# Kernel tuning notes

Hardware: AMD Instinct MI355X
Metric: run time of the kernel (lower is better)

## Reference

```python
import jax, jax.numpy as jnp
import numpy as np

N_U = 50000
N_I = 50000
E = 800000
HID = 64
HEADS = 4
OUT = 32
NEG_SLOPE = 0.2


def _gat(xs, xd, e, ws, wd, a_s, a_d, b, heads, ch, n_dst, concat):
    # xs:[Ns,Fin] xd:[Nd,Fin] e:[2,E]; PyG GATConv (no self loops, eval mode)
    hs = (xs @ ws).reshape(-1, heads, ch)  # [Ns,H,C]
    hd = (xd @ wd).reshape(-1, heads, ch)  # [Nd,H,C]
    al_s = jnp.einsum('nhc,hc->nh', hs, a_s)  # [Ns,H]
    al_d = jnp.einsum('nhc,hc->nh', hd, a_d)  # [Nd,H]
    src, dst = e[0], e[1]
    alpha = jax.nn.leaky_relu(al_s[src] + al_d[dst], NEG_SLOPE)  # [E,H]
    m = jax.lax.stop_gradient(jax.ops.segment_max(alpha, dst, num_segments=n_dst))
    ealpha = jnp.exp(alpha - m[dst])
    denom = jax.ops.segment_sum(ealpha, dst, num_segments=n_dst)
    coef = ealpha / (denom[dst] + 1e-16)  # segment softmax over incoming edges
    msg = hs[src] * coef[:, :, None]  # [E,H,C]
    out = jax.ops.segment_sum(msg, dst, num_segments=n_dst)  # [Nd,H,C]
    out = out.reshape(n_dst, heads * ch) if concat else out.mean(axis=1)
    return out + b


def _forward(x_user, x_item, e_u2i, e_i2u,
             p_user_w, p_user_b, p_item_w, p_item_b,
             l0_u2i_ws, l0_u2i_wd, l0_u2i_as, l0_u2i_ad, l0_u2i_b,
             l0_i2u_ws, l0_i2u_wd, l0_i2u_as, l0_i2u_ad, l0_i2u_b,
             l1_u2i_ws, l1_u2i_wd, l1_u2i_as, l1_u2i_ad, l1_u2i_b,
             l1_i2u_ws, l1_i2u_wd, l1_i2u_as, l1_i2u_ad, l1_i2u_b):
    hu = jax.nn.elu(x_user @ p_user_w + p_user_b)
    hi = jax.nn.elu(x_item @ p_item_w + p_item_b)
    # layer 0: heads=4, concat=True, out dim HID*HEADS; HeteroConv sum (one edge type per dst)
    hi1 = _gat(hu, hi, e_u2i, l0_u2i_ws, l0_u2i_wd, l0_u2i_as, l0_u2i_ad, l0_u2i_b, HEADS, HID, N_I, True)
    hu1 = _gat(hi, hu, e_i2u, l0_i2u_ws, l0_i2u_wd, l0_i2u_as, l0_i2u_ad, l0_i2u_b, HEADS, HID, N_U, True)
    hu1 = jax.nn.elu(hu1)  # dropout is identity in eval mode
    hi1 = jax.nn.elu(hi1)
    # layer 1: heads=1, concat=False -> mean over heads
    hi2 = _gat(hu1, hi1, e_u2i, l1_u2i_ws, l1_u2i_wd, l1_u2i_as, l1_u2i_ad, l1_u2i_b, 1, OUT, N_I, False)
    hu2 = _gat(hi1, hu1, e_i2u, l1_i2u_ws, l1_i2u_wd, l1_i2u_as, l1_i2u_ad, l1_i2u_b, 1, OUT, N_U, False)
    return hu2, hi2


def setup_inputs() -> dict:
    key = jax.random.key(0)
    ks = jax.random.split(key, 32)
    s = 0.1
    d = {
        'x_user': jax.random.normal(ks[0], (N_U, 128), jnp.float32),
        'x_item': jax.random.normal(ks[1], (N_I, 128), jnp.float32),
        'e_u2i': jax.random.randint(ks[2], (2, E), 0, 50000, jnp.int32),
        'e_i2u': jax.random.randint(ks[3], (2, E), 0, 50000, jnp.int32),
        'p_user_w': jax.random.normal(ks[4], (128, HID), jnp.float32) * s,
        'p_user_b': jax.random.normal(ks[5], (HID,), jnp.float32) * s,
        'p_item_w': jax.random.normal(ks[6], (128, HID), jnp.float32) * s,
        'p_item_b': jax.random.normal(ks[7], (HID,), jnp.float32) * s,
    }
    i = 8
    for lname, fin, h, c in (('l0', HID, HEADS, HID), ('l1', HID * HEADS, 1, OUT)):
        for et in ('u2i', 'i2u'):
            odim = h * c if lname == 'l0' else c
            d[f'{lname}_{et}_ws'] = jax.random.normal(ks[i], (fin, h * c), jnp.float32) * s; i += 1
            d[f'{lname}_{et}_wd'] = jax.random.normal(ks[i], (fin, h * c), jnp.float32) * s; i += 1
            d[f'{lname}_{et}_as'] = jax.random.normal(ks[i], (h, c), jnp.float32) * s; i += 1
            d[f'{lname}_{et}_ad'] = jax.random.normal(ks[i], (h, c), jnp.float32) * s; i += 1
            d[f'{lname}_{et}_b'] = jax.random.normal(ks[i], (odim,), jnp.float32) * s; i += 1
    return d


def reference(x_user, x_item, e_u2i, e_i2u,
              p_user_w, p_user_b, p_item_w, p_item_b,
              l0_u2i_ws, l0_u2i_wd, l0_u2i_as, l0_u2i_ad, l0_u2i_b,
              l0_i2u_ws, l0_i2u_wd, l0_i2u_as, l0_i2u_ad, l0_i2u_b,
              l1_u2i_ws, l1_u2i_wd, l1_u2i_as, l1_u2i_ad, l1_u2i_b,
              l1_i2u_ws, l1_i2u_wd, l1_i2u_as, l1_i2u_ad, l1_i2u_b):
    return _forward(x_user, x_item, e_u2i, e_i2u,
                    p_user_w, p_user_b, p_item_w, p_item_b,
                    l0_u2i_ws, l0_u2i_wd, l0_u2i_as, l0_u2i_ad, l0_u2i_b,
                    l0_i2u_ws, l0_i2u_wd, l0_i2u_as, l0_i2u_ad, l0_i2u_b,
                    l1_u2i_ws, l1_u2i_wd, l1_u2i_as, l1_u2i_ad, l1_u2i_b,
                    l1_i2u_ws, l1_i2u_wd, l1_i2u_as, l1_i2u_ad, l1_i2u_b)
```

## Files before the change

### kernel.cpp

```cpp
#include <hip/hip_runtime.h>
#include <cstdint>
#include <cstddef>

#define NN 50000
#define NE 800000
#define GB 196
#define TILE1 4096
#define CAP 8192

typedef __attribute__((ext_vector_type(8))) short short8;
typedef __attribute__((ext_vector_type(4))) float floatx4;

__device__ __forceinline__ float lrelu_f(float x){ return x >= 0.f ? x : 0.2f*x; }
__device__ __forceinline__ float elu_f(float x){ return x > 0.f ? x : __expf(x) - 1.f; }

__device__ __forceinline__ unsigned short f2bf(float f){
  unsigned int u = __float_as_uint(f);
  u += 0x7FFFu + ((u >> 16) & 1u);
  return (unsigned short)(u >> 16);
}
__device__ __forceinline__ float bf2f(unsigned int us){
  return __uint_as_float(us << 16);
}
__device__ __forceinline__ float4 bf4_load(const unsigned short* p){
  uint2 q = *(const uint2*)p;
  return make_float4(bf2f(q.x & 0xffffu), bf2f(q.x >> 16),
                     bf2f(q.y & 0xffffu), bf2f(q.y >> 16));
}
__device__ __forceinline__ uint2 bf4_pack(float4 o){
  uint2 p;
  p.x = (unsigned)f2bf(o.x) | ((unsigned)f2bf(o.y) << 16);
  p.y = (unsigned)f2bf(o.z) | ((unsigned)f2bf(o.w) << 16);
  return p;
}
__device__ __forceinline__ void split_bf(float a, unsigned short& h, unsigned short& l){
  h = f2bf(a);
  l = f2bf(a - bf2f(h));
}

__device__ __forceinline__ float dot2bf(float acc, unsigned a, unsigned b){
  asm("v_dot2_f32_bf16 %0, %1, %2, %0" : "+v"(acc) : "v"(a), "v"(b));
  return acc;
}

__device__ __forceinline__ void agg_pair(float (&acc)[4][8], float (&den)[4],
                                         uint4 q0, uint4 q1, uint2 w0, uint2 w1){
  const unsigned ONE2 = 0x3F803F80u;
  unsigned wp[4];
  wp[0] = __builtin_amdgcn_perm(w1.x, w0.x, 0x05040100u);
  wp[1] = __builtin_amdgcn_perm(w1.x, w0.x, 0x07060302u);
  wp[2] = __builtin_amdgcn_perm(w1.y, w0.y, 0x05040100u);
  wp[3] = __builtin_amdgcn_perm(w1.y, w0.y, 0x07060302u);
  unsigned xp[8];
  xp[0] = __builtin_amdgcn_perm(q1.x, q0.x, 0x05040100u);
  xp[1] = __builtin_amdgcn_perm(q1.x, q0.x, 0x07060302u);
  xp[2] = __builtin_amdgcn_perm(q1.y, q0.y, 0x05040100u);
  xp[3] = __builtin_amdgcn_perm(q1.y, q0.y, 0x07060302u);
  xp[4] = __builtin_amdgcn_perm(q1.z, q0.z, 0x05040100u);
  xp[5] = __builtin_amdgcn_perm(q1.z, q0.z, 0x07060302u);
  xp[6] = __builtin_amdgcn_perm(q1.w, q0.w, 0x05040100u);
  xp[7] = __builtin_amdgcn_perm(q1.w, q0.w, 0x07060302u);
  #pragma unroll
  for (int h=0;h<4;h++){
    den[h] = dot2bf(den[h], wp[h], ONE2);
    #pragma unroll
    for (int c=0;c<8;c++) acc[h][c] = dot2bf(acc[h][c], wp[h], xp[c]);
  }
}

__global__ __launch_bounds__(256) void ghist_kernel(const int* __restrict__ e0,
                                                    const int* __restrict__ e1,
                                                    int* __restrict__ ghist){
  const int ty = blockIdx.y;
  const int* e = ty ? e1 : e0;
  __shared__ int h[GB];
  for (int j=threadIdx.x; j<GB; j+=256) h[j]=0;
  __syncthreads();
  for (int i = blockIdx.x*256 + threadIdx.x; i < NE; i += 256*256)
    atomicAdd(&h[e[NE+i]>>8], 1);
  __syncthreads();
  for (int j=threadIdx.x; j<GB; j+=256) if (h[j]) atomicAdd(&ghist[ty*200+j], h[j]);
}

__global__ __launch_bounds__(256) void gscan_kernel(const int* __restrict__ ghist,
                                                    int* __restrict__ gbase,
                                                    int* __restrict__ gcur){
  __shared__ int wb[4];
  const int t = threadIdx.x, wv = t>>6, l = t&63;
  for (int ty=0; ty<2; ++ty){
    int v = (t < GB) ? ghist[ty*200+t] : 0;
    int sum = v;
    #pragma unroll
    for (int off=1; off<64; off<<=1){
      int x = __shfl_up(sum, off, 64);
      if (l >= off) sum += x;
    }
    if (l == 63) wb[wv] = sum;
    __syncthreads();
    int wbase = 0;
    #pragma unroll
    for (int w=0; w<4; ++w) if (w < wv) wbase += wb[w];
    int excl = wbase + sum - v;
    if (t <= GB) gbase[ty*200+t] = excl;
    if (t <  GB) gcur [ty*200+t] = excl;
    __syncthreads();
  }
}

__global__ __launch_bounds__(256) void part1_kernel(const int* __restrict__ e0,
                                                    const int* __restrict__ e1,
                                                    int* __restrict__ gcur,
                                                    int2* __restrict__ p0,
                                                    int2* __restrict__ p1){
  const int ty = blockIdx.y;
  const int* e = ty ? e1 : e0;
  int2* pairs = ty ? p1 : p0;
  __shared__ int cnt[256];
  __shared__ int lstart[256];
  __shared__ int lcur[256];
  __shared__ int curg[GB];
  __shared__ int lsrc[TILE1];
  __shared__ int ldst[TILE1];
  __shared__ int wb[4];
  const int t = threadIdx.x;
  cnt[t] = 0;
  __syncthreads();
  int dreg[16], sreg[16];
  const int base = blockIdx.x*TILE1;
  const int ntile = min(TILE1, NE - base);
  #pragma unroll
  for (int it=0; it<16; ++it){
    int i = base + it*256 + t;
    int d = -1, s = 0;
    if (i < NE){ d = e[NE+i]; s = e[i]; atomicAdd(&cnt[d>>8], 1); }
    dreg[it] = d; sreg[it] = s;
  }
  __syncthreads();
  int c = cnt[t], sum = c;
  #pragma unroll
  for (int off=1; off<64; off<<=1){
    int x = __shfl_up(sum, off, 64);
    if ((t&63) >= off) sum += x;
  }
  if ((t&63) == 63) wb[t>>6] = sum;
  __syncthreads();
  int wbase = 0;
  #pragma unroll
  for (int w=0; w<4; ++w) if (w < (t>>6)) wbase += wb[w];
  int excl = wbase + sum - c;
  lstart[t] = excl;
  lcur[t] = excl;
  if (t < GB && c > 0) curg[t] = atomicAdd(&gcur[ty*200+t], c);
  __syncthreads();
  #pragma unroll
  for (int it=0; it<16; ++it){
    int d = dreg[it];
    if (d >= 0){
      int pos = atomicAdd(&lcur[d>>8], 1);
      lsrc[pos] = sreg[it];
      ldst[pos] = d;
    }
  }
  __syncthreads();
  for (int i=t; i<ntile; i+=256){
    int d = ldst[i];
    int j = d>>8;
    pairs[curg[j] + (i - lstart[j])] = make_int2(lsrc[i], d);
  }
}

struct Part2Job {
  const int2* pairs; const int* gbase;
  const float* als; const float* ald;
  int* ssrc; int* offs; unsigned short* coef;
};
__global__ __launch_bounds__(256) void part2_kernel(Part2Job j0, Part2Job j1){
  const Part2Job jb = blockIdx.y ? j1 : j0;
  const int b = blockIdx.x;
  const int t = threadIdx.x;
  __shared__ int lcnt[256];
  __shared__ int lcur[256];
  __shared__ int wb[4];
  __shared__ int sorted_src[CAP];
  __shared__ unsigned char sorted_dl[CAP];
  const int gb0 = jb.gbase[b], gb1 = jb.gbase[b+1];
  const int n = gb1 - gb0;
  lcnt[t] = 0;
  __syncthreads();
  for (int i=t; i<n; i+=256)
    atomicAdd(&lcnt[jb.pairs[gb0+i].y - (b<<8)], 1);
  __syncthreads();
  int c = lcnt[t], sum = c;
  #pragma unroll
  for (int off=1; off<64; off<<=1){
    int x = __shfl_up(sum, off, 64);
    if ((t&63) >= off) sum += x;
  }
  if ((t&63) == 63) wb[t>>6] = sum;
  __syncthreads();
  int wbase = 0;
  #pragma unroll
  for (int w=0; w<4; ++w) if (w < (t>>6)) wbase += wb[w];
  int excl = wbase + sum - c;
  lcur[t] = excl;
  int g = (b<<8) + t;
  if (g <= NN) jb.offs[g] = gb0 + excl;
  __syncthreads();
  for (int i=t; i<n; i+=256){
    int2 pr = jb.pairs[gb0+i];
    int dl = pr.y - (b<<8);
    int pos = atomicAdd(&lcur[dl], 1);
    sorted_src[pos] = pr.x;
    sorted_dl[pos] = (unsigned char)dl;
  }
  __syncthreads();
  const float4* als4 = (const float4*)jb.als;
  const float4* ald4 = (const float4*)jb.ald;
  for (int i=t; i<n; i+=256){
    int s  = sorted_src[i];
    int dl = sorted_dl[i];
    float4 a  = als4[s];
    float4 ad = ald4[(b<<8)+dl];
    float4 w;
    w.x = __expf(lrelu_f(a.x+ad.x));
    w.y = __expf(lrelu_f(a.y+ad.y));
    w.z = __expf(lrelu_f(a.z+ad.z));
    w.w = __expf(lrelu_f(a.w+ad.w));
    ((uint2*)jb.coef)[gb0+i] = bf4_pack(w);
    jb.ssrc[gb0+i] = s;
  }
}

struct WcvJob {
  const float* W; const float* cwS; const float* cwD;
  unsigned short* Wth; unsigned short* Wtl;
  int K; int N; int mode;
};
struct WcvArgs { WcvJob j[6]; };
__global__ __launch_bounds__(256) void wconv_kernel(WcvArgs args){
  WcvJob jb = args.j[blockIdx.y];
  int idx = blockIdx.x*256 + threadIdx.x;
  if (idx >= jb.K * jb.N) return;
  int k = idx / jb.N, n = idx % jb.N;
  float val;
  if (jb.mode == 0) val = jb.W[(size_t)k*jb.N + n];
  else {
    if (n < 32)       val = jb.W[(size_t)k*32 + n];
    else if (n == 32) val = jb.cwS[k];
    else if (n == 33) val = jb.cwD[k];
    else              val = 0.f;
  }
  unsigned short h, g;
  split_bf(val, h, g);
  jb.Wth[(size_t)n*jb.K + k] = h;
  jb.Wtl[(size_t)n*jb.K + k] = g;
}

struct MgJob {
  const void* A;
  const unsigned short* Wth;
  const unsigned short* Wtl;
  const float* bias;
  void* C; float* outA; float* outB;
  const float* cwS; const float* cwD;
};
template<int NT, int KK, bool ELU, bool BF16OUT, bool BF16A, bool LG, bool LOGIT>
__global__ __launch_bounds__(256) void mgemm_kernel(MgJob j0, MgJob j1,
                                                    int M, int N)
{
  const MgJob jb = blockIdx.z ? j1 : j0;
  constexpr int TN = NT*16;
  __shared__ __align__(16) unsigned short Ah[64*72];
  __shared__ __align__(16) unsigned short Al[BF16A ? 8 : 64*72];
  __shared__ __align__(16) unsigned short Bh[TN*72];
  __shared__ __align__(16) unsigned short Bl[TN*72];
  __shared__ float CwS[LOGIT ? 256 : 1];
  __shared__ float CwD[LOGIT ? 256 : 1];
  const int t = threadIdx.x;
  const int m0 = blockIdx.x*64;
  const int n0 = blockIdx.y*TN;
  const int wv = t>>6, l = t&63;
  const int lr = l&15, lq = l>>4;
  if constexpr (LOGIT){ CwS[t] = jb.cwS[t]; CwD[t] = jb.cwD[t]; }
  floatx4 acc[NT];
  #pragma unroll
  for (int i=0;i<NT;i++) acc[i] = (floatx4){0.f,0.f,0.f,0.f};

  #pragma unroll
  for (int kt=0; kt<KK; kt+=64){
    if constexpr (BF16A){
      const unsigned short* A = (const unsigned short*)jb.A;
      #pragma unroll
      for (int i=0;i<2;i++){
        int li = t + i*256;
        int r = li >> 3, c8 = (li & 7)*8;
        short8 v = {0,0,0,0,0,0,0,0};
        if (m0 + r < M) v = *(const short8*)(A + (size_t)(m0+r)*KK + kt + c8);
        *(short8*)&Ah[r*72 + c8] = v;
      }
    } else {
      const float* A = (const float*)jb.A;
      #pragma unroll
      for (int i=0;i<4;i++){
        int li = t + i*256;
        int r = li >> 4, c4 = (li & 15)*4;
        float4 v = make_float4(0.f,0.f,0.f,0.f);
        if (m0 + r < M) v = *(const float4*)(A + (size_t)(m0+r)*KK + kt + c4);
        unsigned short h0,h1,h2,h3,g0,g1,g2,g3;
        split_bf(v.x,h0,g0); split_bf(v.y,h1,g1);
        split_bf(v.z,h2,g2); split_bf(v.w,h3,g3);
        uint2 ph = { (unsigned)h0 | ((unsigned)h1<<16), (unsigned)h2 | ((unsigned)h3<<16) };
        uint2 pl = { (unsigned)g0 | ((unsigned)g1<<16), (unsigned)g2 | ((unsigned)g3<<16) };
        *(uint2*)&Ah[r*72 + c4] = ph;
        *(uint2*)&Al[r*72 + c4] = pl;
      }
    }
    for (int c = t; c < TN*8; c += 256){
      int n  = c >> 3;
      int k8 = (c & 7) * 8;
      *(short8*)&Bh[n*72 + k8] =
          *(const short8*)(jb.Wth + (size_t)(n0 + n)*KK + kt + k8);
      *(short8*)&Bl[n*72 + k8] =
          *(const short8*)(jb.Wtl + (size_t)(n0 + n)*KK + kt + k8);
    }
    __syncthreads();
    #pragma unroll
    for (int ks=0; ks<2; ks++){
      const int koff = ks*32 + lq*8;
      short8 a_h = *(const short8*)&Ah[(wv*16+lr)*72 + koff];
      short8 a_l;
      if constexpr (!BF16A) a_l = *(const short8*)&Al[(wv*16+lr)*72 + koff];
      #pragma unroll
      for (int nt=0; nt<NT; nt++){
        short8 b_h = *(const short8*)&Bh[(nt*16+lr)*72 + koff];
        short8 b_l = *(const short8*)&Bl[(nt*16+lr)*72 + koff];
        acc[nt] = __builtin_amdgcn_mfma_f32_16x16x32_bf16(a_h, b_h, acc[nt], 0,0,0);
        acc[nt] = __builtin_amdgcn_mfma_f32_16x16x32_bf16(a_h, b_l, acc[nt], 0,0,0);
        if constexpr (!BF16A)
          acc[nt] = __builtin_amdgcn_mfma_f32_16x16x32_bf16(a_l, b_h, acc[nt], 0,0,0);
      }
    }
    __syncthreads();
  }
  float ls[LOGIT ? 4 : 1][LOGIT ? 4 : 1];
  float ld_[LOGIT ? 4 : 1][LOGIT ? 4 : 1];
  if constexpr (LOGIT){
    #pragma unroll
    for (int r=0;r<4;r++)
      #pragma unroll
      for (int h=0;h<4;h++){ ls[r][h]=0.f; ld_[r][h]=0.f; }
  }
  #pragma unroll
  for (int nt=0; nt<NT; nt++){
    int n = n0 + nt*16 + lr;
    float bv = jb.bias ? jb.bias[n] : 0.f;
    #pragma unroll
    for (int r=0;r<4;r++){
      int m = m0 + wv*16 + lq*4 + r;
      if (m < M){
        float o = acc[nt][r] + bv;
        if (ELU) o = elu_f(o);
        if constexpr (LG){
          if (n < 32)       ((unsigned short*)jb.C)[(size_t)m*32 + n] = f2bf(o);
          else if (n == 32) jb.outA[m] = o;
          else if (n == 33) jb.outB[m] = o;
        } else {
          if (BF16OUT) ((unsigned short*)jb.C)[(size_t)m*N + n] = f2bf(o);
          else         ((float*)jb.C)[(size_t)m*N + n] = o;
        }
        if constexpr (LOGIT){
          #pragma unroll
          for (int h=0;h<4;h++){
            ls[r][h]  = fmaf(o, CwS[h*64 + n], ls[r][h]);
            ld_[r][h] = fmaf(o, CwD[h*64 + n], ld_[r][h]);
          }
        }
      }
    }
  }
  if constexpr (LOGIT){
    #pragma unroll
    for (int r=0;r<4;r++)
      #pragma unroll
      for (int h=0;h<4;h++){
        float a = ls[r][h], d = ld_[r][h];
        #pragma unroll
        for (int off=1; off<16; off<<=1){
          a += __shfl_xor(a, off, 64);
          d += __shfl_xor(d, off, 64);
        }
        ls[r][h]=a; ld_[r][h]=d;
      }
    if (lr == 0){
      #pragma unroll
      for (int r=0;r<4;r++){
        int m = m0 + wv*16 + lq*4 + r;
        if (m < M){
          #pragma unroll
          for (int h=0;h<4;h++){
            jb.outA[(size_t)m*4 + h] = ls[r][h];
            jb.outB[(size_t)m*4 + h] = ld_[r][h];
          }
        }
      }
    }
  }
}

struct HgJob {
  const unsigned short* A;
  const unsigned short* Wth;
  const unsigned short* Wtl;
  const float* den;
  const float* bias; unsigned short* out;
};
__global__ __launch_bounds__(256) void hgemm_kernel(HgJob j0, HgJob j1){
  const HgJob jb = blockIdx.z ? j1 : j0;
  const int head = blockIdx.y;
  const int m0 = blockIdx.x*64;
  __shared__ __align__(16) unsigned short Ah[64*72];
  __shared__ __align__(16) unsigned short Bh[64*72];
  __shared__ __align__(16) unsigned short Bl[64*72];
  const int t = threadIdx.x;
  const int wv = t>>6, l = t&63;
  const int lr = l&15, lq = l>>4;
  floatx4 acc[4];
  #pragma unroll
  for (int i=0;i<4;i++) acc[i] = (floatx4){0.f,0.f,0.f,0.f};
  #pragma unroll
  for (int i=0;i<2;i++){
    int li = t + i*256;
    int r = li >> 3, c8 = (li & 7)*8;
    short8 v = {0,0,0,0,0,0,0,0};
    if (m0 + r < NN) v = *(const short8*)(jb.A + (size_t)(m0+r)*256 + head*64 + c8);
    *(short8*)&Ah[r*72 + c8] = v;
  }
  #pragma unroll
  for (int i=0;i<2;i++){
    int c  = t + i*256;
    int n  = c >> 3;
    int k8 = (c & 7) * 8;
    *(short8*)&Bh[n*72 + k8] =
        *(const short8*)(jb.Wth + (size_t)(head*64 + n)*64 + k8);
    *(short8*)&Bl[n*72 + k8] =
        *(const short8*)(jb.Wtl + (size_t)(head*64 + n)*64 + k8);
  }
  __syncthreads();
  #pragma unroll
  for (int ks=0; ks<2; ks++){
    const int koff = ks*32 + lq*8;
    short8 a_h = *(const short8*)&Ah[(wv*16+lr)*72 + koff];
    #pragma unroll
    for (int nt=0; nt<4; nt++){
      short8 b_h = *(const short8*)&Bh[(nt*16+lr)*72 + koff];
      short8 b_l = *(const short8*)&Bl[(nt*16+lr)*72 + koff];
      acc[nt] = __builtin_amdgcn_mfma_f32_16x16x32_bf16(a_h, b_h, acc[nt], 0,0,0);
      acc[nt] = __builtin_amdgcn_mfma_f32_16x16x32_bf16(a_h, b_l, acc[nt], 0,0,0);
    }
  }
  float inv[4];
  #pragma unroll
  for (int r=0;r<4;r++){
    int m = m0 + wv*16 + lq*4 + r;
    inv[r] = (m < NN) ? 1.f/(jb.den[(size_t)m*4 + head] + 1e-16f) : 0.f;
  }
  #pragma unroll
  for (int nt=0; nt<4; nt++){
    int col = head*64 + nt*16 + lr;
    float bv = jb.bias[col];
    #pragma unroll
    for (int r=0;r<4;r++){
      int m = m0 + wv*16 + lq*4 + r;
      if (m < NN)
        jb.out[(size_t)m*256 + col] = f2bf(elu_f(acc[nt][r]*inv[r] + bv));
    }
  }
}

struct CollapseJob { const float* W; const float* a; float* out; int K,H,C; };
struct CollapseArgs { CollapseJob j[8]; };
__global__ void collapse_kernel(CollapseArgs args){
  CollapseJob jb = args.j[blockIdx.x];
  int t = threadIdx.x;
  if (t < jb.K * jb.H){
    int k = t / jb.H, h = t % jb.H;
    const float* wr = jb.W + (size_t)k * (jb.H*jb.C) + h*jb.C;
    const float* ar = jb.a + h*jb.C;
    float s = 0.f;
    for (int c=0;c<jb.C;c++) s += wr[c]*ar[c];
    jb.out[h*jb.K + k] = s;
  }
}

struct AggPJob {
  const int* offs; const int* ssrc;
  const unsigned short* x;
  const unsigned short* coef;
  unsigned short* agg;
  float* den;
};
__global__ __launch_bounds__(256) void aggpre_kernel(AggPJob ja, AggPJob jbb){
  const AggPJob jb = blockIdx.y ? jbb : ja;
  const int tid = threadIdx.x;
  const int lane = tid & 63, wid = tid >> 6;
  const int grp = lane >> 3;
  const int cl  = lane & 7;
  const int c8  = cl * 8;
  const int dst = blockIdx.x*32 + wid*8 + grp;
  if (dst >= NN) return;
  const int b0 = jb.offs[dst], b1 = jb.offs[dst+1];
  float acc[4][8];
  float den[4] = {0.f,0.f,0.f,0.f};
  #pragma unroll
  for (int h=0;h<4;h++)
    #pragma unroll
    for (int c=0;c<8;c++) acc[h][c]=0.f;
  int e = b0;
  for (; e+3 < b1; e += 4){
    int s0 = jb.ssrc[e];
    int s1 = jb.ssrc[e+1];
    int s2 = jb.ssrc[e+2];
    int s3 = jb.ssrc[e+3];
    uint4 q0 = *(const uint4*)(jb.x + ((size_t)s0<<6) + c8);
    uint4 q1 = *(const uint4*)(jb.x + ((size_t)s1<<6) + c8);
    uint4 q2 = *(const uint4*)(jb.x + ((size_t)s2<<6) + c8);
    uint4 q3 = *(const uint4*)(jb.x + ((size_t)s3<<6) + c8);
    uint2 w0 = *(const uint2*)(jb.coef + (size_t)e*4);
    uint2 w1 = *(const uint2*)(jb.coef + (size_t)(e+1)*4);
    uint2 w2 = *(const uint2*)(jb.coef + (size_t)(e+2)*4);
    uint2 w3 = *(const uint2*)(jb.coef + (size_t)(e+3)*4);
    agg_pair(acc, den, q0, q1, w0, w1);
    agg_pair(acc, den, q2, q3, w2, w3);
  }
  if (e+1 < b1){
    int s0 = jb.ssrc[e];
    int s1 = jb.ssrc[e+1];
    uint4 q0 = *(const uint4*)(jb.x + ((size_t)s0<<6) + c8);
    uint4 q1 = *(const uint4*)(jb.x + ((size_t)s1<<6) + c8);
    uint2 w0 = *(const uint2*)(jb.coef + (size_t)e*4);
    uint2 w1 = *(const uint2*)(jb.coef + (size_t)(e+1)*4);
    agg_pair(acc, den, q0, q1, w0, w1);
    e += 2;
  }
  if (e < b1){
    int s = jb.ssrc[e];
    uint4 q = *(const uint4*)(jb.x + ((size_t)s<<6) + c8);
    uint2 w = *(const uint2*)(jb.coef + (size_t)e*4);
    float wf[4] = { bf2f(w.x & 0xffffu), bf2f(w.x >> 16),
                    bf2f(w.y & 0xffffu), bf2f(w.y >> 16) };
    float xf[8] = { bf2f(q.x & 0xffffu), bf2f(q.x >> 16),
                    bf2f(q.y & 0xffffu), bf2f(q.y >> 16),
                    bf2f(q.z & 0xffffu), bf2f(q.z >> 16),
                    bf2f(q.w & 0xffffu), bf2f(q.w >> 16) };
    #pragma unroll
    for (int h=0;h<4;h++){
      den[h] += wf[h];
      #pragma unroll
      for (int c=0;c<8;c++) acc[h][c] += wf[h]*xf[c];
    }
  }
  #pragma unroll
  for (int h=0;h<4;h++){
    uint2 plo = bf4_pack(make_float4(acc[h][0],acc[h][1],acc[h][2],acc[h][3]));
    uint2 phi = bf4_pack(make_float4(acc[h][4],acc[h][5],acc[h][6],acc[h][7]));
    uint4 pk = { plo.x, plo.y, phi.x, phi.y };
    *(uint4*)(jb.agg + (size_t)dst*256 + h*64 + c8) = pk;
  }
  if (cl == 0)
    *(float4*)(jb.den + (size_t)dst*4) = make_float4(den[0],den[1],den[2],den[3]);
}

struct Agg1Job {
  const int* offs; const int* ssrc;
  const unsigned short* hs;
  const float* als; const float* ald;
  const float* bias; float* out;
};
__global__ __launch_bounds__(256) void agg1_kernel(Agg1Job ja, Agg1Job jbb){
  const Agg1Job jb = blockIdx.y ? jbb : ja;
  const int wid = threadIdx.x>>6, lane = threadIdx.x&63;
  const int dst = blockIdx.x*4 + wid;
  if (dst >= NN) return;
  const int b0 = jb.offs[dst], b1 = jb.offs[dst+1];
  const float ad = jb.ald[dst];
  const int slot = lane>>3, c4 = (lane&7)*4;
  float4 acc = make_float4(0.f,0.f,0.f,0.f);
  float den = 0.f;
  int e = b0 + slot;
  for (; e+8 < b1; e += 16){
    int s0 = jb.ssrc[e], s1 = jb.ssrc[e+8];
    float a0 = jb.als[s0];
    float a1 = jb.als[s1];
    float4 v0 = bf4_load(jb.hs + ((size_t)s0<<5) + c4);
    float4 v1 = bf4_load(jb.hs + ((size_t)s1<<5) + c4);
    float w0 = __expf(lrelu_f(a0 + ad));
    float w1 = __expf(lrelu_f(a1 + ad));
    acc.x += w0*v0.x + w1*v1.x;
    acc.y += w0*v0.y + w1*v1.y;
    acc.z += w0*v0.z + w1*v1.z;
    acc.w += w0*v0.w + w1*v1.w;
    den += w0 + w1;
  }
  if (e < b1){
    int s = jb.ssrc[e];
    float w = __expf(lrelu_f(jb.als[s] + ad));
    float4 v = bf4_load(jb.hs + ((size_t)s<<5) + c4);
    acc.x += w*v.x; acc.y += w*v.y; acc.z += w*v.z; acc.w += w*v.w;
    den += w;
  }
  #pragma unroll
  for (int off=32; off>=8; off>>=1){
    acc.x += __shfl_xor(acc.x, off, 64);
    acc.y += __shfl_xor(acc.y, off, 64);
    acc.z += __shfl_xor(acc.z, off, 64);
    acc.w += __shfl_xor(acc.w, off, 64);
    den   += __shfl_xor(den,   off, 64);
  }
  if (lane < 8){
    const float inv = 1.f/(den + 1e-16f);
    float4 b = *(const float4*)(jb.bias + c4);
    float4 o = make_float4(acc.x*inv+b.x, acc.y*inv+b.y, acc.z*inv+b.z, acc.w*inv+b.w);
    *(float4*)(jb.out + (size_t)dst*32 + c4) = o;
  }
}

extern "C" void kernel_launch(void* const* d_in, const int* in_sizes, int n_in,
                              void* d_out, int out_size, void* d_ws, size_t ws_size,
                              hipStream_t stream)
{
  (void)in_sizes; (void)n_in; (void)out_size; (void)ws_size;
  const float* x_user   = (const float*)d_in[0];
  const float* x_item   = (const float*)d_in[1];
  const int*   e_u2i    = (const int*)  d_in[2];
  const int*   e_i2u    = (const int*)  d_in[3];
  const float* p_user_w = (const float*)d_in[4];
  const float* p_user_b = (const float*)d_in[5];
  const float* p_item_w = (const float*)d_in[6];
  const float* p_item_b = (const float*)d_in[7];
  const float* l0_u2i_ws=(const float*)d_in[8];
  const float* l0_u2i_wd=(const float*)d_in[9];
  const float* l0_u2i_as=(const float*)d_in[10];
  const float* l0_u2i_ad=(const float*)d_in[11];
  const float* l0_u2i_b =(const float*)d_in[12];
  const float* l0_i2u_ws=(const float*)d_in[13];
  const float* l0_i2u_wd=(const float*)d_in[14];
  const float* l0_i2u_as=(const float*)d_in[15];
  const float* l0_i2u_ad=(const float*)d_in[16];
  const float* l0_i2u_b =(const float*)d_in[17];
  const float* l1_u2i_ws=(const float*)d_in[18];
  const float* l1_u2i_wd=(const float*)d_in[19];
  const float* l1_u2i_as=(const float*)d_in[20];
  const float* l1_u2i_ad=(const float*)d_in[21];
  const float* l1_u2i_b =(const float*)d_in[22];
  const float* l1_i2u_ws=(const float*)d_in[23];
  const float* l1_i2u_wd=(const float*)d_in[24];
  const float* l1_i2u_as=(const float*)d_in[25];
  const float* l1_i2u_ad=(const float*)d_in[26];
  const float* l1_i2u_b =(const float*)d_in[27];

  char* base = (char*)d_ws;
  size_t off = 0;
  auto alloc = [&](size_t bytes)->void*{
    void* p = base + off;
    off += (bytes + 255) & ~(size_t)255;
    return p;
  };
  int* offs_u2i = (int*)alloc((size_t)(NN+1)*sizeof(int));
  int* offs_i2u = (int*)alloc((size_t)(NN+1)*sizeof(int));
  int* ssrc_u2i = (int*)alloc((size_t)NE*sizeof(int));
  int* ssrc_i2u = (int*)alloc((size_t)NE*sizeof(int));
  int* ghist    = (int*)alloc((size_t)2*200*sizeof(int));
  int* gbase    = (int*)alloc((size_t)2*200*sizeof(int));
  int* gcur     = (int*)alloc((size_t)2*200*sizeof(int));
  unsigned short* coef0_u2i = (unsigned short*)alloc((size_t)NE*4*sizeof(unsigned short));
  unsigned short* coef0_i2u = (unsigned short*)alloc((size_t)NE*4*sizeof(unsigned short));
  unsigned short* hu = (unsigned short*)alloc((size_t)NN*64*sizeof(unsigned short));
  unsigned short* hi = (unsigned short*)alloc((size_t)NN*64*sizeof(unsigned short));
  unsigned short* agg_u2i = (unsigned short*)alloc((size_t)NN*256*sizeof(unsigned short));
  unsigned short* agg_i2u = (unsigned short*)alloc((size_t)NN*256*sizeof(unsigned short));
  float* den_u2i = (float*)alloc((size_t)NN*4*sizeof(float));
  float* den_i2u = (float*)alloc((size_t)NN*4*sizeof(float));
  unsigned short* hu1 = (unsigned short*)alloc((size_t)NN*256*sizeof(unsigned short));
  unsigned short* hi1 = (unsigned short*)alloc((size_t)NN*256*sizeof(unsigned short));
  unsigned short* hs1_u2i = (unsigned short*)alloc((size_t)NN*32*sizeof(unsigned short));
  unsigned short* hs1_i2u = (unsigned short*)alloc((size_t)NN*32*sizeof(unsigned short));
  float* als0_u2i = (float*)alloc((size_t)NN*4*sizeof(float));
  float* ald0_u2i = (float*)alloc((size_t)NN*4*sizeof(float));
  float* als0_i2u = (float*)alloc((size_t)NN*4*sizeof(float));
  float* ald0_i2u = (float*)alloc((size_t)NN*4*sizeof(float));
  float* als1_u2i = (float*)alloc((size_t)NN*sizeof(float));
  float* ald1_u2i = (float*)alloc((size_t)NN*sizeof(float));
  float* als1_i2u = (float*)alloc((size_t)NN*sizeof(float));
  float* ald1_i2u = (float*)alloc((size_t)NN*sizeof(float));
  float* cw0s_u2i = (float*)alloc(256*sizeof(float));
  float* cw0d_u2i = (float*)alloc(256*sizeof(float));
  float* cw0s_i2u = (float*)alloc(256*sizeof(float));
  float* cw0d_i2u = (float*)alloc(256*sizeof(float));
  float* cw1s_u2i = (float*)alloc(256*sizeof(float));
  float* cw1d_u2i = (float*)alloc(256*sizeof(float));
  float* cw1s_i2u = (float*)alloc(256*sizeof(float));
  float* cw1d_i2u = (float*)alloc(256*sizeof(float));
  unsigned short* wt_pu_h  = (unsigned short*)alloc((size_t)64*128*sizeof(unsigned short));
  unsigned short* wt_pu_l  = (unsigned short*)alloc((size_t)64*128*sizeof(unsigned short));
  unsigned short* wt_pi_h  = (unsigned short*)alloc((size_t)64*128*sizeof(unsigned short));
  unsigned short* wt_pi_l  = (unsigned short*)alloc((size_t)64*128*sizeof(unsigned short));
  unsigned short* wt_l0u_h = (unsigned short*)alloc((size_t)256*64*sizeof(unsigned short));
  unsigned short* wt_l0u_l = (unsigned short*)alloc((size_t)256*64*sizeof(unsigned short));
  unsigned short* wt_l0i_h = (unsigned short*)alloc((size_t)256*64*sizeof(unsigned short));
  unsigned short* wt_l0i_l = (unsigned short*)alloc((size_t)256*64*sizeof(unsigned short));
  unsigned short* wt_wcu_h = (unsigned short*)alloc((size_t)48*256*sizeof(unsigned short));
  unsigned short* wt_wcu_l = (unsigned short*)alloc((size_t)48*256*sizeof(unsigned short));
  unsigned short* wt_wci_h = (unsigned short*)alloc((size_t)48*256*sizeof(unsigned short));
  unsigned short* wt_wci_l = (unsigned short*)alloc((size_t)48*256*sizeof(unsigned short));
  int2* pairs_u2i = (int2*)hu1;
  int2* pairs_i2u = pairs_u2i + NE;

  const int GM = (NN + 63)/64;

  hipMemsetAsync(ghist, 0, (size_t)2*200*sizeof(int), stream);
  ghist_kernel<<<dim3(256,2), 256, 0, stream>>>(e_u2i, e_i2u, ghist);
  gscan_kernel<<<1, 256, 0, stream>>>(ghist, gbase, gcur);
  part1_kernel<<<dim3((NE+TILE1-1)/TILE1,2), 256, 0, stream>>>(
      e_u2i, e_i2u, gcur, pairs_u2i, pairs_i2u);

  CollapseArgs ca;
  ca.j[0] = {l0_u2i_ws, l0_u2i_as, cw0s_u2i, 64, 4, 64};
  ca.j[1] = {l0_u2i_wd, l0_u2i_ad, cw0d_u2i, 64, 4, 64};
  ca.j[2] = {l0_i2u_ws, l0_i2u_as, cw0s_i2u, 64, 4, 64};
  ca.j[3] = {l0_i2u_wd, l0_i2u_ad, cw0d_i2u, 64, 4, 64};
  ca.j[4] = {l1_u2i_ws, l1_u2i_as, cw1s_u2i, 256, 1, 32};
  ca.j[5] = {l1_u2i_wd, l1_u2i_ad, cw1d_u2i, 256, 1, 32};
  ca.j[6] = {l1_i2u_ws, l1_i2u_as, cw1s_i2u, 256, 1, 32};
  ca.j[7] = {l1_i2u_wd, l1_i2u_ad, cw1d_i2u, 256, 1, 32};
  collapse_kernel<<<8, 256, 0, stream>>>(ca);

  WcvArgs wa;
  wa.j[0] = {p_user_w,  nullptr,   nullptr,   wt_pu_h,  wt_pu_l,  128, 64, 0};
  wa.j[1] = {p_item_w,  nullptr,   nullptr,   wt_pi_h,  wt_pi_l,  128, 64, 0};
  wa.j[2] = {l0_u2i_ws, nullptr,   nullptr,   wt_l0u_h, wt_l0u_l, 64, 256, 0};
  wa.j[3] = {l0_i2u_ws, nullptr,   nullptr,   wt_l0i_h, wt_l0i_l, 64, 256, 0};
  wa.j[4] = {l1_u2i_ws, cw1s_u2i,  cw1d_i2u,  wt_wcu_h, wt_wcu_l, 256, 48, 1};
  wa.j[5] = {l1_i2u_ws, cw1s_i2u,  cw1d_u2i,  wt_wci_h, wt_wci_l, 256, 48, 1};
  wconv_kernel<<<dim3(64,6), 256, 0, stream>>>(wa);

  mgemm_kernel<4,128,true,true,false,false,true><<<dim3(GM,1,2), 256, 0, stream>>>(
      MgJob{x_user, wt_pu_h, wt_pu_l, p_user_b, hu, als0_u2i, ald0_i2u, cw0s_u2i, cw0d_i2u},
      MgJob{x_item, wt_pi_h, wt_pi_l, p_item_b, hi, als0_i2u, ald0_u2i, cw0s_i2u, cw0d_u2i},
      NN, 64);

  part2_kernel<<<dim3(GB,2), 256, 0, stream>>>(
      Part2Job{pairs_u2i, gbase,       als0_u2i, ald0_u2i, ssrc_u2i, offs_u2i, coef0_u2i},
      Part2Job{pairs_i2u, gbase + 200, als0_i2u, ald0_i2u, ssrc_i2u, offs_i2u, coef0_i2u});

  aggpre_kernel<<<dim3((NN+31)/32,2), 256, 0, stream>>>(
      AggPJob{offs_u2i, ssrc_u2i, hu, coef0_u2i, agg_u2i, den_u2i},
      AggPJob{offs_i2u, ssrc_i2u, hi, coef0_i2u, agg_i2u, den_i2u});

  hgemm_kernel<<<dim3(GM,4,2), 256, 0, stream>>>(
      HgJob{agg_u2i, wt_l0u_h, wt_l0u_l, den_u2i, l0_u2i_b, hi1},
      HgJob{agg_i2u, wt_l0i_h, wt_l0i_l, den_i2u, l0_i2u_b, hu1});

  mgemm_kernel<3,256,false,true,true,true,false><<<dim3(GM,1,2), 256, 0, stream>>>(
      MgJob{hu1, wt_wcu_h, wt_wcu_l, nullptr, hs1_u2i, als1_u2i, ald1_i2u, nullptr, nullptr},
      MgJob{hi1, wt_wci_h, wt_wci_l, nullptr, hs1_i2u, als1_i2u, ald1_u2i, nullptr, nullptr},
      NN, 48);

  float* hu2 = (float*)d_out;
  float* hi2 = (float*)d_out + (size_t)NN*32;
  agg1_kernel<<<dim3(NN/4,2), 256, 0, stream>>>(
      Agg1Job{offs_u2i, ssrc_u2i, hs1_u2i, als1_u2i, ald1_u2i, l1_u2i_b, hi2},
      Agg1Job{offs_i2u, ssrc_i2u, hs1_i2u, als1_i2u, ald1_i2u, l1_i2u_b, hu2});
}
```

Before: 360.0 us.

## Map eight destination nodes per wavefront in layer-1 aggregation

Changes the layer-1 aggregation kernel so each 8-lane group owns one destination node and walks its edges serially (unrolled by four), instead of a whole wavefront splitting one node's edges across eight slots and then reducing with cross-lane shuffles. This removes the shuffle reduction and the idle lanes on low-degree nodes, and cuts the grid by 8x. In exchange, load balance within a wavefront depends on how degrees vary across the eight nodes it holds.

```diff
diff --git a/kernel.cpp b/kernel.cpp
--- a/kernel.cpp
+++ b/kernel.cpp
@@ -578,50 +578,53 @@
 };
 __global__ __launch_bounds__(256) void agg1_kernel(Agg1Job ja, Agg1Job jbb){
   const Agg1Job jb = blockIdx.y ? jbb : ja;
-  const int wid = threadIdx.x>>6, lane = threadIdx.x&63;
-  const int dst = blockIdx.x*4 + wid;
+  const int tid = threadIdx.x;
+  const int lane = tid & 63, wid = tid >> 6;
+  const int grp = lane >> 3;
+  const int cl  = lane & 7;
+  const int c4  = cl * 4;
+  const int dst = blockIdx.x*32 + wid*8 + grp;
   if (dst >= NN) return;
   const int b0 = jb.offs[dst], b1 = jb.offs[dst+1];
   const float ad = jb.ald[dst];
-  const int slot = lane>>3, c4 = (lane&7)*4;
-  float4 acc = make_float4(0.f,0.f,0.f,0.f);
+  float acc[4] = {0.f,0.f,0.f,0.f};
   float den = 0.f;
-  int e = b0 + slot;
-  for (; e+8 < b1; e += 16){
-    int s0 = jb.ssrc[e], s1 = jb.ssrc[e+8];
+  int e = b0;
+  for (; e+3 < b1; e += 4){
+    int s0 = jb.ssrc[e];
+    int s1 = jb.ssrc[e+1];
+    int s2 = jb.ssrc[e+2];
+    int s3 = jb.ssrc[e+3];
     float a0 = jb.als[s0];
     float a1 = jb.als[s1];
+    float a2 = jb.als[s2];
+    float a3 = jb.als[s3];
     float4 v0 = bf4_load(jb.hs + ((size_t)s0<<5) + c4);
     float4 v1 = bf4_load(jb.hs + ((size_t)s1<<5) + c4);
+    float4 v2 = bf4_load(jb.hs + ((size_t)s2<<5) + c4);
+    float4 v3 = bf4_load(jb.hs + ((size_t)s3<<5) + c4);
     float w0 = __expf(lrelu_f(a0 + ad));
     float w1 = __expf(lrelu_f(a1 + ad));
-    acc.x += w0*v0.x + w1*v1.x;
-    acc.y += w0*v0.y + w1*v1.y;
-    acc.z += w0*v0.z + w1*v1.z;
-    acc.w += w0*v0.w + w1*v1.w;
-    den += w0 + w1;
-  }
-  if (e < b1){
+    float w2 = __expf(lrelu_f(a2 + ad));
+    float w3 = __expf(lrelu_f(a3 + ad));
+    acc[0] += w0*v0.x + w1*v1.x + w2*v2.x + w3*v3.x;
+    acc[1] += w0*v0.y + w1*v1.y + w2*v2.y + w3*v3.y;
+    acc[2] += w0*v0.z + w1*v1.z + w2*v2.z + w3*v3.z;
+    acc[3] += w0*v0.w + w1*v1.w + w2*v2.w + w3*v3.w;
+    den += (w0 + w1) + (w2 + w3);
+  }
+  for (; e < b1; ++e){
     int s = jb.ssrc[e];
     float w = __expf(lrelu_f(jb.als[s] + ad));
     float4 v = bf4_load(jb.hs + ((size_t)s<<5) + c4);
-    acc.x += w*v.x; acc.y += w*v.y; acc.z += w*v.z; acc.w += w*v.w;
+    acc[0] += w*v.x; acc[1] += w*v.y; acc[2] += w*v.z; acc[3] += w*v.w;
     den += w;
   }
-  #pragma unroll
-  for (int off=32; off>=8; off>>=1){
-    acc.x += __shfl_xor(acc.x, off, 64);
-    acc.y += __shfl_xor(acc.y, off, 64);
-    acc.z += __shfl_xor(acc.z, off, 64);
-    acc.w += __shfl_xor(acc.w, off, 64);
-    den   += __shfl_xor(den,   off, 64);
-  }
-  if (lane < 8){
-    const float inv = 1.f/(den + 1e-16f);
-    float4 b = *(const float4*)(jb.bias + c4);
-    float4 o = make_float4(acc.x*inv+b.x, acc.y*inv+b.y, acc.z*inv+b.z, acc.w*inv+b.w);
-    *(float4*)(jb.out + (size_t)dst*32 + c4) = o;
-  }
+  const float inv = 1.f/(den + 1e-16f);
+  float4 b = *(const float4*)(jb.bias + c4);
+  float4 o = make_float4(acc[0]*inv+b.x, acc[1]*inv+b.y,
+                         acc[2]*inv+b.z, acc[3]*inv+b.w);
+  *(float4*)(jb.out + (size_t)dst*32 + c4) = o;
 }
 
 extern "C" void kernel_launch(void* const* d_in, const int* in_sizes, int n_in,
@@ -767,7 +770,7 @@
 
   float* hu2 = (float*)d_out;
   float* hi2 = (float*)d_out + (size_t)NN*32;
-  agg1_kernel<<<dim3(NN/4,2), 256, 0, stream>>>(
+  agg1_kernel<<<dim3((NN+31)/32,2), 256, 0, stream>>>(
       Agg1Job{offs_u2i, ssrc_u2i, hs1_u2i, als1_u2i, ald1_u2i, l1_u2i_b, hi2},
       Agg1Job{offs_i2u, ssrc_i2u, hs1_i2u, als1_i2u, ald1_i2u, l1_i2u_b, hu2});
 }
```

After: 349.3 us. 3.0% less time.
